# Kernel optimization log

Hardware: AMD Instinct MI355X
Metric: run time of the kernel (lower is better)

The kernel has to match this reference:

```python
import jax, jax.numpy as jnp
import numpy as np

N = 50000          # nodes
DEG = 8            # per-node in/out degree
E = N * DEG        # fwd edges (rev = reversed fwd)
H = 128            # hidden_dim
T = 4              # towers
F = H // T         # per-tower F_in (divide_input=True)
FO = H // T        # per-tower F_out
L = 2              # num_layers
IN_DIM = 128
OUT_DIM = 32
AVG_LOG = float(np.log(DEG + 1.0))  # avg of log(deg+1) from deg histogram (all deg==8)
BN_EPS = 1e-5
STD_EPS = 1e-5


def setup_inputs() -> dict:
    key = jax.random.key(0)
    ks = jax.random.split(key, 10)
    x = jax.random.normal(ks[0], (N, IN_DIM), jnp.float32)
    # every node appears exactly DEG times as dst and as src -> deg histogram delta at 8
    dst = jnp.repeat(jnp.arange(N, dtype=jnp.int32), DEG)
    src = jax.random.permutation(ks[1], dst)
    edge_fwd = jnp.stack([src, dst])  # [2, E]

    def rn(k, shape):
        return jax.random.normal(k, shape, jnp.float32) * 0.05

    return dict(
        x=x,
        W_in=rn(ks[2], (IN_DIM, H)), b_in=jnp.zeros((H,), jnp.float32),
        # [layer, relation(fwd/rev), tower, ...]
        pre_W=rn(ks[3], (L, 2, T, 2 * F, F)), pre_b=jnp.zeros((L, 2, T, F), jnp.float32),
        post_W=rn(ks[4], (L, 2, T, 13 * F, FO)), post_b=jnp.zeros((L, 2, T, FO), jnp.float32),
        lin_W=rn(ks[5], (L, 2, H, H)), lin_b=jnp.zeros((L, 2, H), jnp.float32),
        bn_gamma=jnp.ones((L, H), jnp.float32), bn_beta=jnp.zeros((L, H), jnp.float32),
        mlp_W1=rn(ks[6], (H, H)), mlp_b1=jnp.zeros((H,), jnp.float32),
        mlp_W2=rn(ks[7], (H, OUT_DIM)), mlp_b2=jnp.zeros((OUT_DIM,), jnp.float32),
        edge_fwd=edge_fwd,
    )


def _pna(x, src, dst, pre_W, pre_b, post_W, post_b, lin_W, lin_b):
    """One PNAConv (divide_input=True, pre/post_layers=1, no edge attr)."""
    xt = x.reshape(N, T, F)                                   # [N,T,F]
    # message: cat([x_i (dst), x_j (src)]) -> per-tower pre-MLP
    h = jnp.concatenate([xt[dst], xt[src]], axis=-1)          # [E,T,2F]
    m = jnp.einsum('etf,tfg->etg', h, pre_W) + pre_b          # [E,T,F]
    # multi-aggregator scatter reduce over destination nodes
    deg = jax.ops.segment_sum(jnp.ones((m.shape[0],), x.dtype), dst, N)
    degc = jnp.maximum(deg, 1.0)
    inv = (1.0 / degc)[:, None, None]
    mean = jax.ops.segment_sum(m, dst, N) * inv
    mean2 = jax.ops.segment_sum(m * m, dst, N) * inv
    std = jnp.sqrt(jax.nn.relu(mean2 - mean * mean) + STD_EPS)
    mn = jax.ops.segment_min(m, dst, N)
    mx = jax.ops.segment_max(m, dst, N)
    agg = jnp.concatenate([mean, mn, mx, std], axis=-1)       # [N,T,4F]
    # degree scalers: amplification, attenuation, identity
    ld = jnp.log(degc + 1.0)[:, None, None]
    agg = jnp.concatenate([agg * (ld / AVG_LOG), agg * (AVG_LOG / ld), agg], axis=-1)  # [N,T,12F]
    out = jnp.concatenate([xt, agg], axis=-1)                 # [N,T,13F]
    out = jnp.einsum('ntf,tfg->ntg', out, post_W) + post_b    # [N,T,FO]
    out = out.reshape(N, T * FO)
    return out @ lin_W + lin_b                                # [N,H]


def _bn(x, g, b):
    mu = x.mean(0)
    var = x.var(0)  # biased, as torch BatchNorm normalization
    return g * (x - mu) * jax.lax.rsqrt(var + BN_EPS) + b


def reference(x, W_in, b_in, pre_W, pre_b, post_W, post_b, lin_W, lin_b,
              bn_gamma, bn_beta, mlp_W1, mlp_b1, mlp_W2, mlp_b2, edge_fwd):
    src, dst = edge_fwd[0], edge_fwd[1]
    h = jax.nn.relu(x @ W_in + b_in)
    for l in range(L):
        # HeteroConv sum of fwd relation and rev relation (reversed edges)
        y = (_pna(h, src, dst, pre_W[l, 0], pre_b[l, 0], post_W[l, 0], post_b[l, 0], lin_W[l, 0], lin_b[l, 0])
             + _pna(h, dst, src, pre_W[l, 1], pre_b[l, 1], post_W[l, 1], post_b[l, 1], lin_W[l, 1], lin_b[l, 1]))
        h = jax.nn.relu(_bn(y, bn_gamma[l], bn_beta[l]))
        # dropout omitted (deterministic reference / eval mode)
    return jax.nn.relu(h @ mlp_W1 + mlp_b1) @ mlp_W2 + mlp_b2
```

## Files before the change

### kernel.cpp

```cpp
#include <hip/hip_runtime.h>
#include <hip/hip_fp16.h>
#include <cstddef>
#include <cstdint>

#define NN 50000
#define DEG 8
#define EE (NN*DEG)
#define RT_CNT 3125
#define KSTEPS 36
#define W8L 18432
#define MPAD 136

typedef __attribute__((ext_vector_type(8))) short short8;
typedef __attribute__((ext_vector_type(4))) float f32x4;

union Pack8 { __half h[8]; __half2 h2[4]; uint4 u; };
union Pack4 { __half h[4]; uint2 u; };

__global__ void k_build_nbr(const int* __restrict__ ef, int* __restrict__ cnt,
                            int* __restrict__ fwd_nbr, int* __restrict__ rev_nbr) {
    int e = blockIdx.x * blockDim.x + threadIdx.x;
    if (e >= EE) return;
    int s = ef[e], d = ef[EE + e];
    int p = atomicAdd(&cnt[d], 1);
    fwd_nbr[d * DEG + p] = s;
    int q = atomicAdd(&cnt[NN + s], 1);
    rev_nbr[s * DEG + q] = d;
}

__global__ __launch_bounds__(256) void k_wprep(
    const float* __restrict__ post_W, const float* __restrict__ pre_W,
    const float* __restrict__ pre_b, const float* __restrict__ post_b,
    const float* __restrict__ lin_W, const float* __restrict__ lin_b,
    __half* __restrict__ Wcp, float* __restrict__ Qw, float* __restrict__ bc) {
    __shared__ float Pf[160 * 33];
    __shared__ float Wl[32 * 128];
    __shared__ float Wt[32 * 32];
    __shared__ float Ps[32 * 32];
    __shared__ float Q[32 * 32];
    __shared__ float T3s[32];
    int tid = threadIdx.x;
    int m4 = blockIdx.x;
    int l = m4 >> 3, r = (m4 >> 2) & 1, tw = m4 & 3;
    const float* PW = post_W + (size_t)m4 * 416 * 32;
    for (int i = tid; i < 160 * 32; i += 256) {
        int row = i >> 5, g = i & 31;
        float v;
        if (row < 32) v = PW[row * 32 + g];
        else {
            int rr = row - 32;
            v = PW[(32 + rr) * 32 + g] + PW[(160 + rr) * 32 + g] + PW[(288 + rr) * 32 + g];
        }
        Pf[row * 33 + g] = v;
    }
    for (int i = tid; i < 1024; i += 256) Wt[i] = pre_W[(size_t)m4 * 2048 + i];
    for (int i = tid; i < 4096; i += 256)
        Wl[i] = lin_W[(size_t)(l * 2 + r) * 16384 + tw * 32 * 128 + i];
    __syncthreads();
    for (int i = tid; i < 1024; i += 256) {
        int g = i >> 5, j = i & 31;
        Ps[i] = Pf[(32 + g) * 33 + j] + Pf[(64 + g) * 33 + j] + Pf[(96 + g) * 33 + j];
    }
    __syncthreads();
    for (int i = tid; i < 1024; i += 256) {
        int f = i >> 5, j = i & 31;
        float acc = Pf[f * 33 + j];
#pragma unroll
        for (int g = 0; g < 32; g++) acc += Wt[f * 32 + g] * Ps[g * 32 + j];
        Q[i] = acc;
    }
    if (tid < 32) {
        int j = tid;
        float v = post_b[m4 * 32 + j];
#pragma unroll
        for (int g = 0; g < 32; g++) v += pre_b[m4 * 32 + g] * Ps[g * 32 + j];
        T3s[j] = v;
    }
    __syncthreads();
    for (int u = tid; u < 2048; u += 256) {
        int lane = u & 63, t = (u >> 6) & 7, s = u >> 9;
        int quad = lane >> 4, nl = lane & 15;
        int n = t * 16 + nl;
        Pack8 pk;
#pragma unroll
        for (int e = 0; e < 8; e++) {
            int f = quad * 8 + e;
            const float* Pr = &Pf[((s + 1) * 32 + f) * 33];
            float acc = 0.f;
#pragma unroll
            for (int j = 0; j < 32; j++) acc += Pr[j] * Wl[j * 128 + n];
            pk.h[e] = __float2half(acc);
        }
        int ks = 4 + r * 16 + tw * 4 + s;
        *(uint4*)&Wcp[((size_t)l * W8L + (t * KSTEPS + ks) * 64 + lane) * 8] = pk.u;
    }
    for (int i = tid; i < 4096; i += 256) {
        int f = i >> 7, n = i & 127;
        float acc = 0.f;
#pragma unroll
        for (int j = 0; j < 32; j++) acc += Q[f * 32 + j] * Wl[j * 128 + n];
        atomicAdd(&Qw[(size_t)l * 16384 + (tw * 32 + f) * 128 + n], acc);
    }
    if (tid < 128) {
        float v = 0.f;
#pragma unroll
        for (int j = 0; j < 32; j++) v += T3s[j] * Wl[j * 128 + tid];
        atomicAdd(&bc[l * 128 + tid], v);
        if ((m4 & 7) == 0)
            atomicAdd(&bc[l * 128 + tid],
                      lin_b[(2 * l) * 128 + tid] + lin_b[(2 * l + 1) * 128 + tid]);
    }
}

__global__ void k_pack_xt(const float* __restrict__ Qw, __half* __restrict__ Wcp) {
    int gid = blockIdx.x * blockDim.x + threadIdx.x;
    if (gid >= 2 * 4 * 8 * 64) return;
    int lane = gid & 63, t = (gid >> 6) & 7, ks = (gid >> 9) & 3, l = gid >> 11;
    int quad = lane >> 4;
    int n = t * 16 + (lane & 15);
    Pack8 pk;
#pragma unroll
    for (int e = 0; e < 8; e++)
        pk.h[e] = __float2half(Qw[(size_t)l * 16384 + (ks * 32 + quad * 8 + e) * 128 + n]);
    *(uint4*)&Wcp[((size_t)l * W8L + (t * KSTEPS + ks) * 64 + lane) * 8] = pk.u;
}

__global__ void k_pack_b(const float* __restrict__ W, int K, int N,
                         __half* __restrict__ dst) {
    int gid = blockIdx.x * blockDim.x + threadIdx.x;
    int total = (K >> 5) * (N >> 4) * 64;
    if (gid >= total) return;
    int lane = gid & 63;
    int ks = (gid >> 6) % (K >> 5);
    int t = (gid >> 6) / (K >> 5);
    int quad = lane >> 4, nl = lane & 15;
    int n = t * 16 + nl;
    Pack8 pk;
#pragma unroll
    for (int e = 0; e < 8; e++)
        pk.h[e] = __float2half(W[(size_t)(ks * 32 + quad * 8 + e) * N + n]);
    *(uint4*)&dst[(size_t)gid * 8] = pk.u;
}

__global__ __launch_bounds__(256) void k_in_mfma(
    const float* __restrict__ X, const __half* __restrict__ Wp,
    const float* __restrict__ b, float* __restrict__ H) {
    __shared__ __half Sh[4][16 * MPAD];
    int tid = threadIdx.x, wave = tid >> 6, lane = tid & 63;
    int rt = blockIdx.x * 4 + wave;
    if (rt >= RT_CNT) rt = RT_CNT - 1;
    __half* T = Sh[wave];
    const float4* X4 = (const float4*)X + (size_t)rt * 16 * 32;
#pragma unroll
    for (int i = 0; i < 8; i++) {
        int idx = i * 64 + lane;
        int row = idx >> 5, col4 = idx & 31;
        float4 v = X4[idx];
        Pack4 p4;
        p4.h[0] = __float2half(v.x); p4.h[1] = __float2half(v.y);
        p4.h[2] = __float2half(v.z); p4.h[3] = __float2half(v.w);
        *(uint2*)&T[row * MPAD + col4 * 4] = p4.u;
    }
    int mm = lane & 15, quad = lane >> 4;
    short8 a[4];
#pragma unroll
    for (int ks = 0; ks < 4; ks++)
        a[ks] = *(const short8*)&T[mm * MPAD + ks * 32 + quad * 8];
    const short8* Bb = (const short8*)Wp + lane;
    f32x4 acc[8];
#pragma unroll
    for (int t = 0; t < 8; t++) acc[t] = (f32x4){0.f, 0.f, 0.f, 0.f};
#pragma unroll
    for (int ks = 0; ks < 4; ks++)
#pragma unroll
        for (int t = 0; t < 8; t++)
            acc[t] = __builtin_amdgcn_mfma_f32_16x16x32_f16(
                a[ks], Bb[(t * 4 + ks) * 64], acc[t], 0, 0, 0);
#pragma unroll
    for (int t = 0; t < 8; t++) {
        int n = t * 16 + mm;
        float bias = b[n];
#pragma unroll
        for (int r = 0; r < 4; r++) {
            int node = rt * 16 + quad * 4 + r;
            H[(size_t)node * 128 + n] = fmaxf(acc[t][r] + bias, 0.f);
        }
    }
}

template<int BN>
__global__ __launch_bounds__(256) void k_preB(
    const float* __restrict__ Xin, const float* __restrict__ scale,
    const float* __restrict__ shift, float* __restrict__ hout,
    const float* __restrict__ pre_W, int layer, __half* __restrict__ Bplanes) {
    __shared__ float Wb[2 * 4 * 32 * 32];
    __shared__ float Xs[16 * 128];
    int tid = threadIdx.x;
    for (int i = tid; i < 8192; i += 256) {
        int g = i & 31, f = (i >> 5) & 31, t = (i >> 10) & 3, r = i >> 12;
        Wb[i] = pre_W[((((layer * 2 + r) * 4 + t) * 64) + 32 + f) * 32 + g];
    }
    int r = tid >> 7, c = tid & 127, t = c >> 5, g = c & 31;
    const float* wp = &Wb[((r * 4 + t) * 32) * 32 + g];
    int base = blockIdx.x * 16;
    for (int i = tid; i < 16 * 128; i += 256) {
        int col = i & 127;
        size_t gi = (size_t)(base + (i >> 7)) * 128 + col;
        float v = Xin[gi];
        if (BN) {
            v = fmaxf(scale[col] * v + shift[col], 0.f);
            hout[gi] = v;
        }
        Xs[i] = v;
    }
    __syncthreads();
    for (int n = 0; n < 16; n++) {
        float acc = 0.f;
#pragma unroll
        for (int f = 0; f < 32; f++) acc += Xs[n * 128 + t * 32 + f] * wp[f * 32];
        Bplanes[(size_t)r * NN * 128 + (size_t)(base + n) * 128 + c] = __float2half(acc);
    }
}

__global__ __launch_bounds__(256) void k_agg_gemm(
    const float* __restrict__ hbuf, const __half* __restrict__ Bplanes,
    const int* __restrict__ fwd_nbr, const int* __restrict__ rev_nbr,
    const __half* __restrict__ Wcp, const float* __restrict__ bc,
    float* __restrict__ Y, float* __restrict__ bnsum, float* __restrict__ bnsum2) {
    __shared__ __half Spack[KSTEPS * 64 * 8];
    __shared__ float bnred[256];
    int tid = threadIdx.x;
    int blk = blockIdx.x;
    bnred[tid] = 0.f;
    int lane = tid & 63, wv = tid >> 6;
    int m = lane & 15, q = lane >> 4;
    {
        int rel = wv >> 1, twp = (wv & 1) * 2;
        int d = blk * 16 + m;
        const int* nb = (rel ? rev_nbr : fwd_nbr) + d * 8;
        int4 na = ((const int4*)nb)[0], nbv = ((const int4*)nb)[1];
        int idx[8] = {na.x, na.y, na.z, na.w, nbv.x, nbv.y, nbv.z, nbv.w};
        const __half* Bp = Bplanes + (size_t)rel * NN * 128;
#pragma unroll
        for (int t = 0; t < 2; t++) {
            int tw = twp + t;
            Pack8 raw[8];
#pragma unroll
            for (int k = 0; k < 8; k++)
                raw[k].u = *(const uint4*)&Bp[(size_t)idx[k] * 128 + tw * 32 + q * 8];
            float s[8], sq[8], mn[8], mx[8];
#pragma unroll
            for (int j = 0; j < 8; j++) {
                s[j] = 0.f; sq[j] = 0.f; mn[j] = 1e30f; mx[j] = -1e30f;
            }
#pragma unroll
            for (int k = 0; k < 8; k++) {
#pragma unroll
                for (int j = 0; j < 4; j++) {
                    __half2 h = raw[k].h2[j];
                    float a = __half2float(__low2half(h));
                    float b = __half2float(__high2half(h));
                    int j0 = 2 * j, j1 = 2 * j + 1;
                    s[j0] += a; sq[j0] += a * a;
                    mn[j0] = fminf(mn[j0], a); mx[j0] = fmaxf(mx[j0], a);
                    s[j1] += b; sq[j1] += b * b;
                    mn[j1] = fminf(mn[j1], b); mx[j1] = fmaxf(mx[j1], b);
                }
            }
            Pack8 mean, stdv, mnp, mxp;
#pragma unroll
            for (int j = 0; j < 8; j++) {
                float Bm = s[j] * 0.125f;
                mean.h[j] = __float2half(Bm);
                stdv.h[j] = __float2half(
                    sqrtf(fmaxf(sq[j] * 0.125f - Bm * Bm, 0.f) + 1e-5f));
                mnp.h[j] = __float2half(mn[j]);
                mxp.h[j] = __float2half(mx[j]);
            }
            int ksb = 4 + rel * 16 + tw * 4;
            *(uint4*)&Spack[((ksb + 0) * 64 + lane) * 8] = mean.u;
            *(uint4*)&Spack[((ksb + 1) * 64 + lane) * 8] = mnp.u;
            *(uint4*)&Spack[((ksb + 2) * 64 + lane) * 8] = mxp.u;
            *(uint4*)&Spack[((ksb + 3) * 64 + lane) * 8] = stdv.u;
        }
        const float* Hp = &hbuf[(size_t)(blk * 16 + m) * 128 + wv * 32 + q * 8];
        float4 v0 = *(const float4*)Hp;
        float4 v1 = *(const float4*)(Hp + 4);
        Pack8 pk;
        pk.h[0] = __float2half(v0.x); pk.h[1] = __float2half(v0.y);
        pk.h[2] = __float2half(v0.z); pk.h[3] = __float2half(v0.w);
        pk.h[4] = __float2half(v1.x); pk.h[5] = __float2half(v1.y);
        pk.h[6] = __float2half(v1.z); pk.h[7] = __float2half(v1.w);
        *(uint4*)&Spack[(wv * 64 + lane) * 8] = pk.u;
    }
    __syncthreads();
    int t0 = wv * 2;
    const short8* Bb = (const short8*)Wcp + lane;
    f32x4 acc0 = (f32x4){0.f, 0.f, 0.f, 0.f};
    f32x4 acc1 = (f32x4){0.f, 0.f, 0.f, 0.f};
    short8 b0 = Bb[(size_t)(t0 * KSTEPS) * 64];
    short8 b1 = Bb[(size_t)((t0 + 1) * KSTEPS) * 64];
#pragma unroll 4
    for (int ks = 0; ks < KSTEPS; ks++) {
        short8 a = *(const short8*)&Spack[(ks * 64 + lane) * 8];
        int n1 = (ks + 1 < KSTEPS) ? ks + 1 : 0;
        short8 nb0 = Bb[((size_t)t0 * KSTEPS + n1) * 64];
        short8 nb1 = Bb[(((size_t)t0 + 1) * KSTEPS + n1) * 64];
        acc0 = __builtin_amdgcn_mfma_f32_16x16x32_f16(a, b0, acc0, 0, 0, 0);
        acc1 = __builtin_amdgcn_mfma_f32_16x16x32_f16(a, b1, acc1, 0, 0, 0);
        b0 = nb0; b1 = nb1;
    }
    int nl = lane & 15, quad = lane >> 4;
#pragma unroll
    for (int tt = 0; tt < 2; tt++) {
        f32x4 acc = tt ? acc1 : acc0;
        int n = (t0 + tt) * 16 + nl;
        float bias = bc[n];
        float ls = 0.f, ls2 = 0.f;
#pragma unroll
        for (int r = 0; r < 4; r++) {
            float v = acc[r] + bias;
            int node = blk * 16 + quad * 4 + r;
            Y[(size_t)node * 128 + n] = v;
            ls += v; ls2 += v * v;
        }
        ls += __shfl_xor(ls, 16); ls += __shfl_xor(ls, 32);
        ls2 += __shfl_xor(ls2, 16); ls2 += __shfl_xor(ls2, 32);
        if (quad == 0) { bnred[n] += ls; bnred[128 + n] += ls2; }
    }
    __syncthreads();
    if (tid < 128) {
        atomicAdd(&bnsum[tid], bnred[tid]);
        atomicAdd(&bnsum2[tid], bnred[128 + tid]);
    }
}

__global__ void k_bn_final(const float* __restrict__ bnsum, const float* __restrict__ bnsum2,
                           const float* __restrict__ gamma, const float* __restrict__ beta,
                           int layer, float* __restrict__ scale, float* __restrict__ shift) {
    int c = threadIdx.x;
    float mu = bnsum[c] * (1.f / NN);
    float var = bnsum2[c] * (1.f / NN) - mu * mu;
    float sc = gamma[layer * 128 + c] * rsqrtf(var + 1e-5f);
    scale[c] = sc;
    shift[c] = beta[layer * 128 + c] - mu * sc;
}

__global__ __launch_bounds__(256) void k_mlp_mfma(
    const float* __restrict__ Yb, const float* __restrict__ scale,
    const float* __restrict__ shift, const __half* __restrict__ W1p,
    const float* __restrict__ b1, const __half* __restrict__ W2p,
    const float* __restrict__ b2, float* __restrict__ out) {
    __shared__ __half Sh[4][16 * MPAD];
    int tid = threadIdx.x, wave = tid >> 6, lane = tid & 63;
    int rt = blockIdx.x * 4 + wave;
    if (rt >= RT_CNT) rt = RT_CNT - 1;
    __half* T = Sh[wave];
    const float4* Y4 = (const float4*)Yb + (size_t)rt * 16 * 32;
    const float4* sc4 = (const float4*)scale;
    const float4* sh4 = (const float4*)shift;
#pragma unroll
    for (int i = 0; i < 8; i++) {
        int idx = i * 64 + lane;
        int row = idx >> 5, col4 = idx & 31;
        float4 v = Y4[idx];
        float4 s = sc4[col4], f = sh4[col4];
        Pack4 p4;
        p4.h[0] = __float2half(fmaxf(s.x * v.x + f.x, 0.f));
        p4.h[1] = __float2half(fmaxf(s.y * v.y + f.y, 0.f));
        p4.h[2] = __float2half(fmaxf(s.z * v.z + f.z, 0.f));
        p4.h[3] = __float2half(fmaxf(s.w * v.w + f.w, 0.f));
        *(uint2*)&T[row * MPAD + col4 * 4] = p4.u;
    }
    int mm = lane & 15, quad = lane >> 4;
    short8 a[4];
#pragma unroll
    for (int ks = 0; ks < 4; ks++)
        a[ks] = *(const short8*)&T[mm * MPAD + ks * 32 + quad * 8];
    const short8* B1 = (const short8*)W1p + lane;
    f32x4 acc[8];
#pragma unroll
    for (int t = 0; t < 8; t++) acc[t] = (f32x4){0.f, 0.f, 0.f, 0.f};
#pragma unroll
    for (int ks = 0; ks < 4; ks++)
#pragma unroll
        for (int t = 0; t < 8; t++)
            acc[t] = __builtin_amdgcn_mfma_f32_16x16x32_f16(
                a[ks], B1[(t * 4 + ks) * 64], acc[t], 0, 0, 0);
#pragma unroll
    for (int t = 0; t < 8; t++) {
        int n = t * 16 + mm;
        float bias = b1[n];
#pragma unroll
        for (int r = 0; r < 4; r++)
            T[(quad * 4 + r) * MPAD + n] = __float2half(fmaxf(acc[t][r] + bias, 0.f));
    }
    short8 a2[4];
#pragma unroll
    for (int ks = 0; ks < 4; ks++)
        a2[ks] = *(const short8*)&T[mm * MPAD + ks * 32 + quad * 8];
    const short8* B2 = (const short8*)W2p + lane;
    f32x4 acc2[2];
#pragma unroll
    for (int t = 0; t < 2; t++) acc2[t] = (f32x4){0.f, 0.f, 0.f, 0.f};
#pragma unroll
    for (int ks = 0; ks < 4; ks++)
#pragma unroll
        for (int t = 0; t < 2; t++)
            acc2[t] = __builtin_amdgcn_mfma_f32_16x16x32_f16(
                a2[ks], B2[(t * 4 + ks) * 64], acc2[t], 0, 0, 0);
#pragma unroll
    for (int t = 0; t < 2; t++) {
        int n = t * 16 + mm;
        float bias = b2[n];
#pragma unroll
        for (int r = 0; r < 4; r++)
            out[(size_t)(rt * 16 + quad * 4 + r) * 32 + n] = acc2[t][r] + bias;
    }
}

extern "C" void kernel_launch(void* const* d_in, const int* in_sizes, int n_in,
                              void* d_out, int out_size, void* d_ws, size_t ws_size,
                              hipStream_t stream) {
    const float* x      = (const float*)d_in[0];
    const float* W_in   = (const float*)d_in[1];
    const float* b_in   = (const float*)d_in[2];
    const float* pre_W  = (const float*)d_in[3];
    const float* pre_b  = (const float*)d_in[4];
    const float* post_W = (const float*)d_in[5];
    const float* post_b = (const float*)d_in[6];
    const float* lin_W  = (const float*)d_in[7];
    const float* lin_b  = (const float*)d_in[8];
    const float* bn_g   = (const float*)d_in[9];
    const float* bn_b   = (const float*)d_in[10];
    const float* mlp_W1 = (const float*)d_in[11];
    const float* mlp_b1 = (const float*)d_in[12];
    const float* mlp_W2 = (const float*)d_in[13];
    const float* mlp_b2 = (const float*)d_in[14];
    const int*   edge   = (const int*)d_in[15];
    float* out = (float*)d_out;

    char* w = (char*)d_ws;
    const size_t plane = (size_t)NN * 128 * sizeof(float);
    float* hbuf = (float*)w; w += plane;
    float* ybuf = (float*)w; w += plane;
    __half* Bpl = (__half*)w; w += plane;
    int* fwd_nbr = (int*)w; w += (size_t)NN * DEG * sizeof(int);
    int* rev_nbr = (int*)w; w += (size_t)NN * DEG * sizeof(int);
    int* cnt     = (int*)w; w += (size_t)2 * NN * sizeof(int);
    float* Qw    = (float*)w; w += (size_t)2 * 128 * 128 * sizeof(float);
    float* bc    = (float*)w; w += 2 * 128 * sizeof(float);
    __half* Wcp  = (__half*)w; w += (size_t)2 * KSTEPS * 32 * 128 * sizeof(__half);
    __half* Winp = (__half*)w; w += (size_t)128 * 128 * sizeof(__half);
    __half* W1p  = (__half*)w; w += (size_t)128 * 128 * sizeof(__half);
    __half* W2p  = (__half*)w; w += (size_t)128 * 32 * sizeof(__half);
    float* bnsum  = (float*)w; w += 128 * sizeof(float);
    float* bnsum2 = (float*)w; w += 128 * sizeof(float);
    float* scale  = (float*)w; w += 128 * sizeof(float);
    float* shift  = (float*)w; w += 128 * sizeof(float);

    const int gWave = (RT_CNT + 3) / 4;

    (void)hipMemsetAsync(cnt, 0, (size_t)2 * NN * sizeof(int), stream);
    (void)hipMemsetAsync(Qw, 0, (size_t)(2 * 128 * 128 + 2 * 128) * sizeof(float), stream);
    k_build_nbr<<<(EE + 255) / 256, 256, 0, stream>>>(edge, cnt, fwd_nbr, rev_nbr);
    k_wprep<<<16, 256, 0, stream>>>(post_W, pre_W, pre_b, post_b, lin_W, lin_b,
                                    Wcp, Qw, bc);
    k_pack_xt<<<16, 256, 0, stream>>>(Qw, Wcp);
    k_pack_b<<<8, 256, 0, stream>>>(W_in, 128, 128, Winp);
    k_pack_b<<<8, 256, 0, stream>>>(mlp_W1, 128, 128, W1p);
    k_pack_b<<<2, 256, 0, stream>>>(mlp_W2, 128, 32, W2p);

    k_in_mfma<<<gWave, 256, 0, stream>>>(x, Winp, b_in, hbuf);

    for (int l = 0; l < 2; l++) {
        if (l == 0)
            k_preB<0><<<RT_CNT, 256, 0, stream>>>(hbuf, nullptr, nullptr, nullptr,
                                                  pre_W, 0, Bpl);
        else
            k_preB<1><<<RT_CNT, 256, 0, stream>>>(ybuf, scale, shift, hbuf,
                                                  pre_W, 1, Bpl);
        (void)hipMemsetAsync(bnsum, 0, 2 * 128 * sizeof(float), stream);
        k_agg_gemm<<<RT_CNT, 256, 0, stream>>>(
            hbuf, Bpl, fwd_nbr, rev_nbr, Wcp + (size_t)l * KSTEPS * 32 * 128,
            bc + l * 128, ybuf, bnsum, bnsum2);
        k_bn_final<<<1, 128, 0, stream>>>(bnsum, bnsum2, bn_g, bn_b, l, scale, shift);
    }

    k_mlp_mfma<<<gWave, 256, 0, stream>>>(ybuf, scale, shift, W1p, mlp_b1,
                                          W2p, mlp_b2, out);
}
```

Before: 481.2 us.

## Remap gather to full-row lanes, swizzle LDS packing, deepen weight prefetch

Each wave now handles 4 destination nodes and gathers full 256-byte neighbour rows, loading both relations up front instead of quarter-row strided loads per relation and tower. The aggregate tiles are written to LDS with an XOR-swizzled position, and the MFMA loop reads them back with the matching inverse mapping. The weight fragments are prefetched six k-steps ahead in a register ring, the main loop is fully unrolled, and launch bounds request 4 blocks per CU. This targets gather memory coalescing and global-load latency in the GEMM, at the cost of more registers and more complex indexing.

Result: faster. 458.3 us (-4.8%).

```diff
diff --git a/kernel.cpp b/kernel.cpp
--- a/kernel.cpp
+++ b/kernel.cpp
@@ -222,7 +222,7 @@
     }
 }
 
-__global__ __launch_bounds__(256) void k_agg_gemm(
+__global__ __launch_bounds__(256, 4) void k_agg_gemm(
     const float* __restrict__ hbuf, const __half* __restrict__ Bplanes,
     const int* __restrict__ fwd_nbr, const int* __restrict__ rev_nbr,
     const __half* __restrict__ Wcp, const float* __restrict__ bc,
@@ -233,84 +233,100 @@
     int blk = blockIdx.x;
     bnred[tid] = 0.f;
     int lane = tid & 63, wv = tid >> 6;
-    int m = lane & 15, q = lane >> 4;
+    int s = lane >> 4, f16 = lane & 15;
+    int tw = f16 >> 2, quad = f16 & 3;
+    int m = wv * 4 + s;
+    int d = blk * 16 + m;
     {
-        int rel = wv >> 1, twp = (wv & 1) * 2;
-        int d = blk * 16 + m;
-        const int* nb = (rel ? rev_nbr : fwd_nbr) + d * 8;
-        int4 na = ((const int4*)nb)[0], nbv = ((const int4*)nb)[1];
-        int idx[8] = {na.x, na.y, na.z, na.w, nbv.x, nbv.y, nbv.z, nbv.w};
-        const __half* Bp = Bplanes + (size_t)rel * NN * 128;
-#pragma unroll
-        for (int t = 0; t < 2; t++) {
-            int tw = twp + t;
-            Pack8 raw[8];
-#pragma unroll
-            for (int k = 0; k < 8; k++)
-                raw[k].u = *(const uint4*)&Bp[(size_t)idx[k] * 128 + tw * 32 + q * 8];
-            float s[8], sq[8], mn[8], mx[8];
+        const int4* nf = (const int4*)&fwd_nbr[d * 8];
+        const int4* nr = (const int4*)&rev_nbr[d * 8];
+        int4 a0 = nf[0], a1 = nf[1], b0v = nr[0], b1v = nr[1];
+        int idx0[8] = {a0.x, a0.y, a0.z, a0.w, a1.x, a1.y, a1.z, a1.w};
+        int idx1[8] = {b0v.x, b0v.y, b0v.z, b0v.w, b1v.x, b1v.y, b1v.z, b1v.w};
+        int fo = f16 * 8;
+        Pack8 r0[8], r1[8];
+        const __half* Bp1 = Bplanes + (size_t)NN * 128;
+#pragma unroll
+        for (int k = 0; k < 8; k++)
+            r0[k].u = *(const uint4*)&Bplanes[(size_t)idx0[k] * 128 + fo];
+#pragma unroll
+        for (int k = 0; k < 8; k++)
+            r1[k].u = *(const uint4*)&Bp1[(size_t)idx1[k] * 128 + fo];
+        const float* Hp = &hbuf[(size_t)(blk * 16 + f16) * 128 + wv * 32 + s * 8];
+        float4 xv0 = *(const float4*)Hp;
+        float4 xv1 = *(const float4*)(Hp + 4);
+        int pos = 16 * quad + (m ^ quad ^ ((tw & 1) << 2));
+#pragma unroll
+        for (int rel = 0; rel < 2; rel++) {
+            Pack8* rr = rel ? r1 : r0;
+            float sS[8], qS[8], mnS[8], mxS[8];
 #pragma unroll
             for (int j = 0; j < 8; j++) {
-                s[j] = 0.f; sq[j] = 0.f; mn[j] = 1e30f; mx[j] = -1e30f;
+                sS[j] = 0.f; qS[j] = 0.f; mnS[j] = 1e30f; mxS[j] = -1e30f;
             }
 #pragma unroll
             for (int k = 0; k < 8; k++) {
 #pragma unroll
-                for (int j = 0; j < 4; j++) {
-                    __half2 h = raw[k].h2[j];
+                for (int j2 = 0; j2 < 4; j2++) {
+                    __half2 h = rr[k].h2[j2];
                     float a = __half2float(__low2half(h));
                     float b = __half2float(__high2half(h));
-                    int j0 = 2 * j, j1 = 2 * j + 1;
-                    s[j0] += a; sq[j0] += a * a;
-                    mn[j0] = fminf(mn[j0], a); mx[j0] = fmaxf(mx[j0], a);
-                    s[j1] += b; sq[j1] += b * b;
-                    mn[j1] = fminf(mn[j1], b); mx[j1] = fmaxf(mx[j1], b);
+                    int j0 = 2 * j2, j1 = j0 + 1;
+                    sS[j0] += a; qS[j0] += a * a;
+                    mnS[j0] = fminf(mnS[j0], a); mxS[j0] = fmaxf(mxS[j0], a);
+                    sS[j1] += b; qS[j1] += b * b;
+                    mnS[j1] = fminf(mnS[j1], b); mxS[j1] = fmaxf(mxS[j1], b);
                 }
             }
             Pack8 mean, stdv, mnp, mxp;
 #pragma unroll
             for (int j = 0; j < 8; j++) {
-                float Bm = s[j] * 0.125f;
+                float Bm = sS[j] * 0.125f;
                 mean.h[j] = __float2half(Bm);
                 stdv.h[j] = __float2half(
-                    sqrtf(fmaxf(sq[j] * 0.125f - Bm * Bm, 0.f) + 1e-5f));
-                mnp.h[j] = __float2half(mn[j]);
-                mxp.h[j] = __float2half(mx[j]);
+                    sqrtf(fmaxf(qS[j] * 0.125f - Bm * Bm, 0.f) + 1e-5f));
+                mnp.h[j] = __float2half(mnS[j]);
+                mxp.h[j] = __float2half(mxS[j]);
             }
             int ksb = 4 + rel * 16 + tw * 4;
-            *(uint4*)&Spack[((ksb + 0) * 64 + lane) * 8] = mean.u;
-            *(uint4*)&Spack[((ksb + 1) * 64 + lane) * 8] = mnp.u;
-            *(uint4*)&Spack[((ksb + 2) * 64 + lane) * 8] = mxp.u;
-            *(uint4*)&Spack[((ksb + 3) * 64 + lane) * 8] = stdv.u;
-        }
-        const float* Hp = &hbuf[(size_t)(blk * 16 + m) * 128 + wv * 32 + q * 8];
-        float4 v0 = *(const float4*)Hp;
-        float4 v1 = *(const float4*)(Hp + 4);
+            *(uint4*)&Spack[((size_t)(ksb + 0) * 64 + pos) * 8] = mean.u;
+            *(uint4*)&Spack[((size_t)(ksb + 1) * 64 + pos) * 8] = mnp.u;
+            *(uint4*)&Spack[((size_t)(ksb + 2) * 64 + pos) * 8] = mxp.u;
+            *(uint4*)&Spack[((size_t)(ksb + 3) * 64 + pos) * 8] = stdv.u;
+        }
+        int posx = 16 * s + (f16 ^ s ^ ((wv & 1) << 2));
         Pack8 pk;
-        pk.h[0] = __float2half(v0.x); pk.h[1] = __float2half(v0.y);
-        pk.h[2] = __float2half(v0.z); pk.h[3] = __float2half(v0.w);
-        pk.h[4] = __float2half(v1.x); pk.h[5] = __float2half(v1.y);
-        pk.h[6] = __float2half(v1.z); pk.h[7] = __float2half(v1.w);
-        *(uint4*)&Spack[(wv * 64 + lane) * 8] = pk.u;
+        pk.h[0] = __float2half(xv0.x); pk.h[1] = __float2half(xv0.y);
+        pk.h[2] = __float2half(xv0.z); pk.h[3] = __float2half(xv0.w);
+        pk.h[4] = __float2half(xv1.x); pk.h[5] = __float2half(xv1.y);
+        pk.h[6] = __float2half(xv1.z); pk.h[7] = __float2half(xv1.w);
+        *(uint4*)&Spack[((size_t)wv * 64 + posx) * 8] = pk.u;
     }
     __syncthreads();
+    int mB = lane & 15, qB = lane >> 4;
     int t0 = wv * 2;
     const short8* Bb = (const short8*)Wcp + lane;
     f32x4 acc0 = (f32x4){0.f, 0.f, 0.f, 0.f};
     f32x4 acc1 = (f32x4){0.f, 0.f, 0.f, 0.f};
-    short8 b0 = Bb[(size_t)(t0 * KSTEPS) * 64];
-    short8 b1 = Bb[(size_t)((t0 + 1) * KSTEPS) * 64];
-#pragma unroll 4
+    short8 p0[6], p1[6];
+#pragma unroll
+    for (int dd = 0; dd < 6; dd++) {
+        p0[dd] = Bb[((size_t)t0 * KSTEPS + dd) * 64];
+        p1[dd] = Bb[((size_t)(t0 + 1) * KSTEPS + dd) * 64];
+    }
+#pragma unroll
     for (int ks = 0; ks < KSTEPS; ks++) {
-        short8 a = *(const short8*)&Spack[(ks * 64 + lane) * 8];
-        int n1 = (ks + 1 < KSTEPS) ? ks + 1 : 0;
-        short8 nb0 = Bb[((size_t)t0 * KSTEPS + n1) * 64];
-        short8 nb1 = Bb[(((size_t)t0 + 1) * KSTEPS + n1) * 64];
-        acc0 = __builtin_amdgcn_mfma_f32_16x16x32_f16(a, b0, acc0, 0, 0, 0);
-        acc1 = __builtin_amdgcn_mfma_f32_16x16x32_f16(a, b1, acc1, 0, 0, 0);
-        b0 = nb0; b1 = nb1;
-    }
-    int nl = lane & 15, quad = lane >> 4;
+        int twk = (ks < 4) ? ks : (((ks - 4) >> 2) & 3);
+        int pos = 16 * qB + (mB ^ qB ^ ((twk & 1) << 2));
+        short8 a = *(const short8*)&Spack[((size_t)ks * 64 + pos) * 8];
+        acc0 = __builtin_amdgcn_mfma_f32_16x16x32_f16(a, p0[ks % 6], acc0, 0, 0, 0);
+        acc1 = __builtin_amdgcn_mfma_f32_16x16x32_f16(a, p1[ks % 6], acc1, 0, 0, 0);
+        if (ks + 6 < KSTEPS) {
+            p0[ks % 6] = Bb[((size_t)t0 * KSTEPS + ks + 6) * 64];
+            p1[ks % 6] = Bb[((size_t)(t0 + 1) * KSTEPS + ks + 6) * 64];
+        }
+    }
+    int nl = lane & 15, qd = lane >> 4;
 #pragma unroll
     for (int tt = 0; tt < 2; tt++) {
         f32x4 acc = tt ? acc1 : acc0;
@@ -320,13 +336,13 @@
 #pragma unroll
         for (int r = 0; r < 4; r++) {
             float v = acc[r] + bias;
-            int node = blk * 16 + quad * 4 + r;
+            int node = blk * 16 + qd * 4 + r;
             Y[(size_t)node * 128 + n] = v;
             ls += v; ls2 += v * v;
         }
         ls += __shfl_xor(ls, 16); ls += __shfl_xor(ls, 32);
         ls2 += __shfl_xor(ls2, 16); ls2 += __shfl_xor(ls2, 32);
-        if (quad == 0) { bnred[n] += ls; bnred[128 + n] += ls2; }
+        if (qd == 0) { bnred[n] += ls; bnred[128 + n] += ls2; }
     }
     __syncthreads();
     if (tid < 128) {
```
